# Performance work log

Hardware: AMD Instinct MI355X
Metric: run time of the kernel (lower is better)

Reference implementation:

```python
import jax, jax.numpy as jnp
import numpy as np

OUT, IN, R = 8192, 8192, 16
GROUP = 16
SCALING = 16.0 / 16.0  # lora_alpha / r
# nvfp4 (e2m1) code table: 3 low bits magnitude, bit 3 = sign
NVFP4_LUT = jnp.array([0.0, 0.5, 1.0, 1.5, 2.0, 3.0, 4.0, 6.0,
                       -0.0, -0.5, -1.0, -1.5, -2.0, -3.0, -4.0, -6.0],
                      dtype=jnp.float32)


def setup_inputs() -> dict:
    key = jax.random.key(0)
    k1, k2, k3, k4, k5 = jax.random.split(key, 5)
    x = jax.random.normal(k1, (64, IN), dtype=jnp.float32)
    packed_weight = jax.random.randint(k2, (OUT, IN // 2), 0, 256, dtype=jnp.int32).astype(jnp.uint8)
    # effective block scales (global scale already absorbed, as in _load_prequantized_nvfp4)
    weight_block_scales = (jax.random.uniform(k3, (OUT, IN // GROUP), dtype=jnp.float32) + 0.1) * 0.01
    lora_A = jax.random.normal(k4, (R, IN), dtype=jnp.float32) * (1.0 / np.sqrt(IN))
    lora_B = jax.random.normal(k5, (OUT, R), dtype=jnp.float32) * 0.01
    return {"x": x, "packed_weight": packed_weight,
            "weight_block_scales": weight_block_scales,
            "lora_A": lora_A, "lora_B": lora_B}


def _dequant_nvfp4(packed, block_scales):
    # packed: (OUT, IN//2) uint8, two fp4 codes per byte (low nibble = even index)
    low = (packed & 0xF).astype(jnp.int32)
    high = (packed >> 4).astype(jnp.int32)
    codes = jnp.stack([low, high], axis=-1).reshape(packed.shape[0], -1)  # (OUT, IN)
    vals = NVFP4_LUT[codes]
    O, I = vals.shape
    # per-block scale over groups of GROUP along in_features
    W = (vals.reshape(O, I // GROUP, GROUP) * block_scales[:, :, None]).reshape(O, I)
    return W


def reference(x, packed_weight, weight_block_scales, lora_A, lora_B):
    W = _dequant_nvfp4(packed_weight, weight_block_scales)      # (OUT, IN) fp32
    base = x @ W.T                                              # (B, OUT)
    lora = (x @ lora_A.T) @ lora_B.T                            # (B, OUT)
    return base + SCALING * lora
```

## Files before the change

kernel.cpp:

```cpp
#include <hip/hip_runtime.h>
#include <stdint.h>

#define IN_F   8192
#define OUT_F  8192
#define MB     64
#define RANK   16
#define KSPLIT 16

typedef _Float16 f16x8 __attribute__((ext_vector_type(8)));
typedef _Float16 f16x2 __attribute__((ext_vector_type(2)));
typedef float    f32x4 __attribute__((ext_vector_type(4)));

__device__ __forceinline__ unsigned pk2h(float a, float b) {
    return __builtin_bit_cast(unsigned, __builtin_amdgcn_cvt_pkrtz(a, b));
}

__device__ __forceinline__ f16x8 decode8(unsigned p, unsigned s2) {
    unsigned q  = p >> 4;
    unsigned me = __builtin_amdgcn_perm(0x46444240u, 0x3E3C3800u, p & 0x07070707u);
    unsigned mo = __builtin_amdgcn_perm(0x46444240u, 0x3E3C3800u, q & 0x07070707u);
    unsigned he = ((p & 0x08080808u) << 4) | me;
    unsigned ho = ((q & 0x08080808u) << 4) | mo;
    unsigned bu0 = __builtin_amdgcn_perm(ho, he, 0x040C000Cu);
    unsigned bu1 = __builtin_amdgcn_perm(ho, he, 0x050C010Cu);
    unsigned bu2 = __builtin_amdgcn_perm(ho, he, 0x060C020Cu);
    unsigned bu3 = __builtin_amdgcn_perm(ho, he, 0x070C030Cu);
    f16x2 sv = __builtin_bit_cast(f16x2, s2);
    f16x2 h0 = __builtin_bit_cast(f16x2, bu0) * sv;
    f16x2 h1 = __builtin_bit_cast(f16x2, bu1) * sv;
    f16x2 h2 = __builtin_bit_cast(f16x2, bu2) * sv;
    f16x2 h3 = __builtin_bit_cast(f16x2, bu3) * sv;
    f16x8 b;
    b[0]=h0[0]; b[1]=h0[1]; b[2]=h1[0]; b[3]=h1[1];
    b[4]=h2[0]; b[5]=h2[1]; b[6]=h3[0]; b[7]=h3[1];
    return b;
}

__device__ __forceinline__ unsigned pack4(uint4 a) {
    unsigned t0 = __builtin_amdgcn_perm(a.y, a.x, 0x0C0C0400u);
    unsigned t1 = __builtin_amdgcn_perm(a.w, a.z, 0x0C0C0400u);
    return __builtin_amdgcn_perm(t1, t0, 0x05040100u);
}

__global__ __launch_bounds__(256) void prep_kernel(
    const float* __restrict__ x, const float* __restrict__ lora_A,
    uint2* __restrict__ xf2, float* __restrict__ tp)
{
    const int m = blockIdx.x, kq = blockIdx.y;
    const int tid = threadIdx.x;
    const int mt = m >> 4, l15 = m & 15;
    float acc[RANK];
#pragma unroll
    for (int r = 0; r < RANK; ++r) acc[r] = 0.f;

    const float4* x4 = (const float4*)(x + (size_t)m * IN_F);
    const float4* A4 = (const float4*)lora_A;
#pragma unroll
    for (int it = 0; it < 2; ++it) {
        int j = kq * 512 + it * 256 + tid;
        float4 xv = x4[j];
        uint2 u;
        u.x = pk2h(xv.x, xv.y);
        u.y = pk2h(xv.z, xv.w);
        int kstep = j >> 3, quad = (j >> 1) & 3, h = j & 1;
        xf2[(size_t)(((kstep * 4 + mt) * 64 + quad * 16 + l15) * 2 + h)] = u;
#pragma unroll
        for (int r = 0; r < RANK; ++r) {
            float4 av = A4[(size_t)r * (IN_F / 4) + j];
            acc[r] += xv.x * av.x + xv.y * av.y + xv.z * av.z + xv.w * av.w;
        }
    }
#pragma unroll
    for (int r = 0; r < RANK; ++r)
#pragma unroll
        for (int off = 32; off > 0; off >>= 1)
            acc[r] += __shfl_down(acc[r], off);

    __shared__ float red[4][RANK];
    int lane = tid & 63, wid = tid >> 6;
    if (lane == 0) {
#pragma unroll
        for (int r = 0; r < RANK; ++r) red[wid][r] = acc[r];
    }
    __syncthreads();
    if (tid < RANK)
        tp[((size_t)kq * MB + m) * RANK + tid] =
            red[0][tid] + red[1][tid] + red[2][tid] + red[3][tid];
}

__device__ __forceinline__ float4 lora4(const float* __restrict__ tp, int m,
                                        const float* __restrict__ lora_B, int n4) {
    float ta[RANK];
#pragma unroll
    for (int r = 0; r < RANK; ++r) ta[r] = 0.f;
#pragma unroll
    for (int kq = 0; kq < 4; ++kq) {
        const float4* t4 = (const float4*)(tp + ((size_t)kq * MB + m) * RANK);
#pragma unroll
        for (int i = 0; i < 4; ++i) {
            float4 v = t4[i];
            ta[4*i+0] += v.x; ta[4*i+1] += v.y; ta[4*i+2] += v.z; ta[4*i+3] += v.w;
        }
    }
    float4 o;
    float* op = (float*)&o;
#pragma unroll
    for (int j = 0; j < 4; ++j) {
        const float4* B4 = (const float4*)(lora_B + (size_t)(n4 + j) * RANK);
        float s = 0.f;
#pragma unroll
        for (int i = 0; i < 4; ++i) {
            float4 b = B4[i];
            s += ta[4*i+0]*b.x + ta[4*i+1]*b.y + ta[4*i+2]*b.z + ta[4*i+3]*b.w;
        }
        op[j] = s;
    }
    return o;
}

__global__ __launch_bounds__(256) void lora_kernel(
    const float* __restrict__ tp, const float* __restrict__ lora_B,
    float* __restrict__ out)
{
    const int gid = blockIdx.x * 256 + threadIdx.x;
    ((float4*)out)[gid] = lora4(tp, gid >> 11, lora_B, (gid & 2047) * 4);
}

__global__ __launch_bounds__(256) void finish_kernel(
    const float* __restrict__ partial, const float* __restrict__ tp,
    const float* __restrict__ lora_B, float* __restrict__ out)
{
    const int gid = blockIdx.x * 256 + threadIdx.x;
    float4 p = {0.f, 0.f, 0.f, 0.f};
#pragma unroll
    for (int ksp = 0; ksp < KSPLIT; ++ksp) {
        float4 v = ((const float4*)partial)[(size_t)ksp * (MB * OUT_F / 4) + gid];
        p.x += v.x; p.y += v.y; p.z += v.z; p.w += v.w;
    }
    float4 l = lora4(tp, gid >> 11, lora_B, (gid & 2047) * 4);
    p.x += l.x; p.y += l.y; p.z += l.z; p.w += l.w;
    ((float4*)out)[gid] = p;
}

template<int ATOMIC>
__global__ __launch_bounds__(256, 3) void main4_kernel(
    const void*  __restrict__ Wpv,
    const float* __restrict__ scales,
    const uint4* __restrict__ xf4,
    float*       __restrict__ dst)
{
    __shared__ __align__(16) unsigned wbuf[2][2048];

    const int tid = threadIdx.x;
    const int lane = tid & 63, w = tid >> 6;
    const int l15 = lane & 15, quad = lane >> 4, qh = quad >> 1;
    const int ks = blockIdx.x, by = blockIdx.y;
    const int n0 = by * 128 + w * 32;
    const int row = n0 + l15;

    unsigned dv = ((const unsigned*)Wpv)[lane];
    const bool fmt1 = (__ballot(dv > 255u) == 0ull);

    unsigned sreg[2][16];
#pragma unroll
    for (int nt = 0; nt < 2; ++nt) {
        const float4* sp = (const float4*)(scales + (size_t)(row + nt * 16) * (IN_F / 16)
                                           + ks * 32);
#pragma unroll
        for (int i = 0; i < 8; ++i) {
            float4 vv = sp[i];
            float a = qh ? vv.y : vv.x, b = qh ? vv.w : vv.z;
            sreg[nt][2 * i]     = pk2h(a, a);
            sreg[nt][2 * i + 1] = pk2h(b, b);
        }
    }

    f32x4 acc[4][2];
#pragma unroll
    for (int mt = 0; mt < 4; ++mt)
#pragma unroll
        for (int nt = 0; nt < 2; ++nt)
            acc[mt][nt] = (f32x4){0.f, 0.f, 0.f, 0.f};

    const uint4* xp  = xf4 + (size_t)ks * 4096 + lane;
    const uint4* Wp4 = (const uint4*)Wpv;

    uint4 rg[8];

#define LOADC(c)                                                              \
    do {                                                                      \
        if (fmt1) {                                                           \
            _Pragma("unroll") for (int i = 0; i < 8; ++i) {                   \
                int rl = (tid >> 4) + i * 16;                                 \
                rg[i] = Wp4[(size_t)(by * 128 + rl) * 1024                    \
                            + (ks * 64 + (c) * 16 + (tid & 15))];             \
            }                                                                 \
        } else {                                                              \
            _Pragma("unroll") for (int i = 0; i < 2; ++i) {                   \
                int rl = (tid >> 2) + i * 64;                                 \
                rg[i] = Wp4[(size_t)(by * 128 + rl) * 256                     \
                            + (ks * 16 + (c) * 4 + (tid & 3))];               \
            }                                                                 \
        }                                                                     \
    } while (0)

#define WRITEC(buf)                                                           \
    do {                                                                      \
        if (fmt1) {                                                           \
            int te = tid & 15;                                                \
            _Pragma("unroll") for (int i = 0; i < 8; ++i) {                   \
                int rl = (tid >> 4) + i * 16;                                 \
                wbuf[buf][rl * 16 + (te ^ (rl & 14))] = pack4(rg[i]);         \
            }                                                                 \
        } else {                                                              \
            _Pragma("unroll") for (int i = 0; i < 2; ++i) {                   \
                int rl = (tid >> 2) + i * 64;                                 \
                int eb = (tid & 3) * 4;                                       \
                wbuf[buf][rl * 16 + ((eb + 0) ^ (rl & 14))] = rg[i].x;        \
                wbuf[buf][rl * 16 + ((eb + 1) ^ (rl & 14))] = rg[i].y;        \
                wbuf[buf][rl * 16 + ((eb + 2) ^ (rl & 14))] = rg[i].z;        \
                wbuf[buf][rl * 16 + ((eb + 3) ^ (rl & 14))] = rg[i].w;        \
            }                                                                 \
        }                                                                     \
    } while (0)

    LOADC(0);
    WRITEC(0);
    __syncthreads();
    LOADC(1);

#pragma unroll
    for (int c = 0; c < 4; ++c) {
#pragma unroll
        for (int sc = 0; sc < 4; ++sc) {
            const int s = c * 4 + sc;
            f16x8 afr[4];
#pragma unroll
            for (int mt = 0; mt < 4; ++mt)
                afr[mt] = __builtin_bit_cast(f16x8, xp[(s * 4 + mt) * 64]);
#pragma unroll
            for (int nt = 0; nt < 2; ++nt) {
                const int rl = w * 32 + nt * 16 + l15;
                unsigned p = wbuf[c & 1][rl * 16 + ((sc * 4 + quad) ^ (l15 & 14))];
                f16x8 b = decode8(p, sreg[nt][s]);
#pragma unroll
                for (int mt = 0; mt < 4; ++mt)
                    acc[mt][nt] = __builtin_amdgcn_mfma_f32_16x16x32_f16(
                        afr[mt], b, acc[mt][nt], 0, 0, 0);
            }
        }
        if (c < 3) {
            __syncthreads();
            WRITEC((c + 1) & 1);
            if (c < 2) LOADC(c + 2);
            __syncthreads();
        }
    }
#undef LOADC
#undef WRITEC

    if (ATOMIC == 0) {
        float* pb = dst + (size_t)ks * (MB * OUT_F);
#pragma unroll
        for (int mt = 0; mt < 4; ++mt)
#pragma unroll
            for (int nt = 0; nt < 2; ++nt)
#pragma unroll
                for (int r = 0; r < 4; ++r)
                    pb[(size_t)(mt * 16 + quad * 4 + r) * OUT_F + n0 + nt * 16 + l15]
                        = acc[mt][nt][r];
    } else {
#pragma unroll
        for (int mt = 0; mt < 4; ++mt)
#pragma unroll
            for (int nt = 0; nt < 2; ++nt)
#pragma unroll
                for (int r = 0; r < 4; ++r)
                    atomicAdd(&dst[(size_t)(mt * 16 + quad * 4 + r) * OUT_F
                                   + n0 + nt * 16 + l15], acc[mt][nt][r]);
    }
}

extern "C" void kernel_launch(void* const* d_in, const int* in_sizes, int n_in,
                              void* d_out, int out_size, void* d_ws, size_t ws_size,
                              hipStream_t stream)
{
    (void)in_sizes; (void)n_in; (void)out_size;
    const float* x      = (const float*)d_in[0];
    const void*  Wp     = (const void*)d_in[1];
    const float* scales = (const float*)d_in[2];
    const float* lora_A = (const float*)d_in[3];
    const float* lora_B = (const float*)d_in[4];
    float* out = (float*)d_out;

    char* ws = (char*)d_ws;
    float* tp      = (float*)ws;
    uint2* xf      = (uint2*)(ws + 65536);
    float* partial = (float*)(ws + (2u << 20));
    const bool full = ws_size >= ((size_t)34 << 20);

    prep_kernel<<<dim3(64, 4), 256, 0, stream>>>(x, lora_A, xf, tp);

    if (full) {
        main4_kernel<0><<<dim3(KSPLIT, 64), 256, 0, stream>>>(
            Wp, scales, (const uint4*)xf, partial);
        finish_kernel<<<(MB * OUT_F / 4) / 256, 256, 0, stream>>>(
            partial, tp, lora_B, out);
    } else {
        lora_kernel<<<(MB * OUT_F / 4) / 256, 256, 0, stream>>>(tp, lora_B, out);
        main4_kernel<1><<<dim3(KSPLIT, 64), 256, 0, stream>>>(
            Wp, scales, (const uint4*)xf, out);
    }
}
```

Before: 239.8 us.

## Stage activations in LDS and use per-wave weight buffers without block barriers

The kernel now copies the block's whole activation slice into shared memory once, so the MMA loop reads A fragments from LDS instead of global memory. Each wave loads, repacks and reads its own weight rows through a private double-buffered LDS region. This removes the block-wide __syncthreads in the K loop and relies on manual s_waitcnt with two register stages to overlap loads. LDS use rises to about 80KB per block and the launch bound drops to 2 blocks per CU, cutting occupancy. The hand-coded waitcnt values and the lack of intra-wave LDS sync risk subtle ordering bugs.

After: 235.3 us. Within noise of the previous version (-1.9%).

```diff
diff --git a/kernel.cpp b/kernel.cpp
--- a/kernel.cpp
+++ b/kernel.cpp
@@ -14,6 +14,8 @@
 __device__ __forceinline__ unsigned pk2h(float a, float b) {
     return __builtin_bit_cast(unsigned, __builtin_amdgcn_cvt_pkrtz(a, b));
 }
+
+#define MEMBAR() __asm__ __volatile__("" ::: "memory")
 
 __device__ __forceinline__ f16x8 decode8(unsigned p, unsigned s2) {
     unsigned q  = p >> 4;
@@ -143,13 +145,14 @@
 }
 
 template<int ATOMIC>
-__global__ __launch_bounds__(256, 3) void main4_kernel(
+__global__ __launch_bounds__(256, 2) void main5_kernel(
     const void*  __restrict__ Wpv,
     const float* __restrict__ scales,
     const uint4* __restrict__ xf4,
     float*       __restrict__ dst)
 {
-    __shared__ __align__(16) unsigned wbuf[2][2048];
+    __shared__ __align__(16) uint4    xs[4096];
+    __shared__ __align__(16) unsigned wpk[4][2][512];
 
     const int tid = threadIdx.x;
     const int lane = tid & 63, w = tid >> 6;
@@ -175,89 +178,110 @@
         }
     }
 
-    f32x4 acc[4][2];
-#pragma unroll
-    for (int mt = 0; mt < 4; ++mt)
-#pragma unroll
-        for (int nt = 0; nt < 2; ++nt)
-            acc[mt][nt] = (f32x4){0.f, 0.f, 0.f, 0.f};
-
-    const uint4* xp  = xf4 + (size_t)ks * 4096 + lane;
     const uint4* Wp4 = (const uint4*)Wpv;
-
-    uint4 rg[8];
-
-#define LOADC(c)                                                              \
+    uint4 rg[2][8];
+
+#define LOADW(c, p)                                                           \
     do {                                                                      \
         if (fmt1) {                                                           \
             _Pragma("unroll") for (int i = 0; i < 8; ++i) {                   \
-                int rl = (tid >> 4) + i * 16;                                 \
-                rg[i] = Wp4[(size_t)(by * 128 + rl) * 1024                    \
-                            + (ks * 64 + (c) * 16 + (tid & 15))];             \
+                int idx = i * 64 + lane;                                      \
+                int r = idx >> 4, col = idx & 15;                             \
+                rg[p][i] = Wp4[(size_t)(n0 + r) * 1024                        \
+                               + (ks * 64 + (c) * 16 + col)];                 \
             }                                                                 \
         } else {                                                              \
             _Pragma("unroll") for (int i = 0; i < 2; ++i) {                   \
-                int rl = (tid >> 2) + i * 64;                                 \
-                rg[i] = Wp4[(size_t)(by * 128 + rl) * 256                     \
-                            + (ks * 16 + (c) * 4 + (tid & 3))];               \
+                int idx = i * 64 + lane;                                      \
+                int r = idx >> 2, u = idx & 3;                                \
+                rg[p][i] = Wp4[(size_t)(n0 + r) * 256                         \
+                               + (ks * 16 + (c) * 4 + u)];                    \
             }                                                                 \
         }                                                                     \
     } while (0)
 
-#define WRITEC(buf)                                                           \
+#define WRITEW(c, p)                                                          \
     do {                                                                      \
+        unsigned* wb = &wpk[w][(c) & 1][0];                                   \
         if (fmt1) {                                                           \
-            int te = tid & 15;                                                \
             _Pragma("unroll") for (int i = 0; i < 8; ++i) {                   \
-                int rl = (tid >> 4) + i * 16;                                 \
-                wbuf[buf][rl * 16 + (te ^ (rl & 14))] = pack4(rg[i]);         \
+                int idx = i * 64 + lane;                                      \
+                int r = idx >> 4, dcol = idx & 15;                            \
+                wb[r * 16 + (dcol & 3) * 4 + (dcol >> 2)] = pack4(rg[p][i]);  \
             }                                                                 \
         } else {                                                              \
             _Pragma("unroll") for (int i = 0; i < 2; ++i) {                   \
-                int rl = (tid >> 2) + i * 64;                                 \
-                int eb = (tid & 3) * 4;                                       \
-                wbuf[buf][rl * 16 + ((eb + 0) ^ (rl & 14))] = rg[i].x;        \
-                wbuf[buf][rl * 16 + ((eb + 1) ^ (rl & 14))] = rg[i].y;        \
-                wbuf[buf][rl * 16 + ((eb + 2) ^ (rl & 14))] = rg[i].z;        \
-                wbuf[buf][rl * 16 + ((eb + 3) ^ (rl & 14))] = rg[i].w;        \
+                int idx = i * 64 + lane;                                      \
+                int r = idx >> 2, u = idx & 3;                                \
+                wb[r * 16 + 0 * 4 + u] = rg[p][i].x;                          \
+                wb[r * 16 + 1 * 4 + u] = rg[p][i].y;                          \
+                wb[r * 16 + 2 * 4 + u] = rg[p][i].z;                          \
+                wb[r * 16 + 3 * 4 + u] = rg[p][i].w;                          \
             }                                                                 \
         }                                                                     \
     } while (0)
 
-    LOADC(0);
-    WRITEC(0);
+    uint4 xr[16];
+    {
+        const uint4* gsrc = xf4 + (size_t)ks * 4096;
+#pragma unroll
+        for (int i = 0; i < 16; ++i) xr[i] = gsrc[i * 256 + tid];
+    }
+    LOADW(0, 0);
+    LOADW(1, 1);
+#pragma unroll
+    for (int i = 0; i < 16; ++i) xs[i * 256 + tid] = xr[i];
     __syncthreads();
-    LOADC(1);
+
+    f32x4 acc[4][2];
+#pragma unroll
+    for (int mt = 0; mt < 4; ++mt)
+#pragma unroll
+        for (int nt = 0; nt < 2; ++nt)
+            acc[mt][nt] = (f32x4){0.f, 0.f, 0.f, 0.f};
+
+    MEMBAR();
+    __builtin_amdgcn_s_waitcnt(0x0F78);
+    MEMBAR();
+    WRITEW(0, 0);
 
 #pragma unroll
     for (int c = 0; c < 4; ++c) {
+        const uint4* wb4 = (const uint4*)&wpk[w][c & 1][0];
+        uint4 b0 = wb4[(0 * 16 + l15) * 4 + quad];
+        uint4 b1 = wb4[(1 * 16 + l15) * 4 + quad];
 #pragma unroll
         for (int sc = 0; sc < 4; ++sc) {
             const int s = c * 4 + sc;
             f16x8 afr[4];
 #pragma unroll
             for (int mt = 0; mt < 4; ++mt)
-                afr[mt] = __builtin_bit_cast(f16x8, xp[(s * 4 + mt) * 64]);
-#pragma unroll
-            for (int nt = 0; nt < 2; ++nt) {
-                const int rl = w * 32 + nt * 16 + l15;
-                unsigned p = wbuf[c & 1][rl * 16 + ((sc * 4 + quad) ^ (l15 & 14))];
-                f16x8 b = decode8(p, sreg[nt][s]);
-#pragma unroll
-                for (int mt = 0; mt < 4; ++mt)
-                    acc[mt][nt] = __builtin_amdgcn_mfma_f32_16x16x32_f16(
-                        afr[mt], b, acc[mt][nt], 0, 0, 0);
-            }
+                afr[mt] = __builtin_bit_cast(f16x8, xs[(s * 4 + mt) * 64 + lane]);
+            const unsigned pw0 = sc == 0 ? b0.x : sc == 1 ? b0.y : sc == 2 ? b0.z : b0.w;
+            const unsigned pw1 = sc == 0 ? b1.x : sc == 1 ? b1.y : sc == 2 ? b1.z : b1.w;
+            f16x8 bb0 = decode8(pw0, sreg[0][s]);
+#pragma unroll
+            for (int mt = 0; mt < 4; ++mt)
+                acc[mt][0] = __builtin_amdgcn_mfma_f32_16x16x32_f16(
+                    afr[mt], bb0, acc[mt][0], 0, 0, 0);
+            f16x8 bb1 = decode8(pw1, sreg[1][s]);
+#pragma unroll
+            for (int mt = 0; mt < 4; ++mt)
+                acc[mt][1] = __builtin_amdgcn_mfma_f32_16x16x32_f16(
+                    afr[mt], bb1, acc[mt][1], 0, 0, 0);
         }
         if (c < 3) {
-            __syncthreads();
-            WRITEC((c + 1) & 1);
-            if (c < 2) LOADC(c + 2);
-            __syncthreads();
-        }
-    }
-#undef LOADC
-#undef WRITEC
+            MEMBAR();
+            if (c < 2) LOADW(c + 2, c & 1);
+            MEMBAR();
+            if (c < 2) { __builtin_amdgcn_s_waitcnt(0x0F78); }
+            else       { __builtin_amdgcn_s_waitcnt(0x0F70); }
+            MEMBAR();
+            WRITEW(c + 1, (c + 1) & 1);
+        }
+    }
+#undef LOADW
+#undef WRITEW
 
     if (ATOMIC == 0) {
         float* pb = dst + (size_t)ks * (MB * OUT_F);
@@ -302,13 +326,13 @@
     prep_kernel<<<dim3(64, 4), 256, 0, stream>>>(x, lora_A, xf, tp);
 
     if (full) {
-        main4_kernel<0><<<dim3(KSPLIT, 64), 256, 0, stream>>>(
+        main5_kernel<0><<<dim3(KSPLIT, 64), 256, 0, stream>>>(
             Wp, scales, (const uint4*)xf, partial);
         finish_kernel<<<(MB * OUT_F / 4) / 256, 256, 0, stream>>>(
             partial, tp, lora_B, out);
     } else {
         lora_kernel<<<(MB * OUT_F / 4) / 256, 256, 0, stream>>>(tp, lora_B, out);
-        main4_kernel<1><<<dim3(KSPLIT, 64), 256, 0, stream>>>(
+        main5_kernel<1><<<dim3(KSPLIT, 64), 256, 0, stream>>>(
             Wp, scales, (const uint4*)xf, out);
     }
 }
```

## Restructure main kernel: whole K-slab in LDS, fewer k-splits, narrower N tiles

Applied to the files above, without the earlier changes.

The main kernel now splits K only four ways. Each block covers 64 output rows and loads its full 2048-wide K slab of packed weights and block scales into LDS in one pass, replacing the double-buffered chunk pipeline. Each wave computes one 16-column N tile over 64 MFMA steps, and scales are read per step from LDS rather than held in registers. This cuts partial-sum workspace and finish-kernel reduction traffic by a factor of four, at the cost of about 80KB of LDS per block, no overlap between weight loading and compute, and lower occupancy.

Result: no change. 236.6 us (-1.3%).

```diff
diff --git a/kernel.cpp b/kernel.cpp
--- a/kernel.cpp
+++ b/kernel.cpp
@@ -5,7 +5,7 @@
 #define OUT_F  8192
 #define MB     64
 #define RANK   16
-#define KSPLIT 16
+#define KSPLIT 4
 
 typedef _Float16 f16x8 __attribute__((ext_vector_type(8)));
 typedef _Float16 f16x2 __attribute__((ext_vector_type(2)));
@@ -143,141 +143,100 @@
 }
 
 template<int ATOMIC>
-__global__ __launch_bounds__(256, 3) void main4_kernel(
+__global__ __launch_bounds__(256, 2) void main6_kernel(
     const void*  __restrict__ Wpv,
     const float* __restrict__ scales,
     const uint4* __restrict__ xf4,
     float*       __restrict__ dst)
 {
-    __shared__ __align__(16) unsigned wbuf[2][2048];
+    __shared__ __align__(16) unsigned wlds[64 * 256];
+    __shared__ __align__(16) unsigned slds[64 * 64];
 
     const int tid = threadIdx.x;
     const int lane = tid & 63, w = tid >> 6;
     const int l15 = lane & 15, quad = lane >> 4, qh = quad >> 1;
-    const int ks = blockIdx.x, by = blockIdx.y;
-    const int n0 = by * 128 + w * 32;
-    const int row = n0 + l15;
+    const int ksp = blockIdx.x, by = blockIdx.y;
+    const int nb = by * 64;
+    const int rw = w * 16 + l15;
 
     unsigned dv = ((const unsigned*)Wpv)[lane];
     const bool fmt1 = (__ballot(dv > 255u) == 0ull);
 
-    unsigned sreg[2][16];
-#pragma unroll
-    for (int nt = 0; nt < 2; ++nt) {
-        const float4* sp = (const float4*)(scales + (size_t)(row + nt * 16) * (IN_F / 16)
-                                           + ks * 32);
-#pragma unroll
-        for (int i = 0; i < 8; ++i) {
-            float4 vv = sp[i];
-            float a = qh ? vv.y : vv.x, b = qh ? vv.w : vv.z;
-            sreg[nt][2 * i]     = pk2h(a, a);
-            sreg[nt][2 * i + 1] = pk2h(b, b);
-        }
-    }
-
-    f32x4 acc[4][2];
-#pragma unroll
-    for (int mt = 0; mt < 4; ++mt)
-#pragma unroll
-        for (int nt = 0; nt < 2; ++nt)
-            acc[mt][nt] = (f32x4){0.f, 0.f, 0.f, 0.f};
-
-    const uint4* xp  = xf4 + (size_t)ks * 4096 + lane;
     const uint4* Wp4 = (const uint4*)Wpv;
 
-    uint4 rg[8];
-
-#define LOADC(c)                                                              \
-    do {                                                                      \
-        if (fmt1) {                                                           \
-            _Pragma("unroll") for (int i = 0; i < 8; ++i) {                   \
-                int rl = (tid >> 4) + i * 16;                                 \
-                rg[i] = Wp4[(size_t)(by * 128 + rl) * 1024                    \
-                            + (ks * 64 + (c) * 16 + (tid & 15))];             \
-            }                                                                 \
-        } else {                                                              \
-            _Pragma("unroll") for (int i = 0; i < 2; ++i) {                   \
-                int rl = (tid >> 2) + i * 64;                                 \
-                rg[i] = Wp4[(size_t)(by * 128 + rl) * 256                     \
-                            + (ks * 16 + (c) * 4 + (tid & 3))];               \
-            }                                                                 \
-        }                                                                     \
-    } while (0)
-
-#define WRITEC(buf)                                                           \
-    do {                                                                      \
-        if (fmt1) {                                                           \
-            int te = tid & 15;                                                \
-            _Pragma("unroll") for (int i = 0; i < 8; ++i) {                   \
-                int rl = (tid >> 4) + i * 16;                                 \
-                wbuf[buf][rl * 16 + (te ^ (rl & 14))] = pack4(rg[i]);         \
-            }                                                                 \
-        } else {                                                              \
-            _Pragma("unroll") for (int i = 0; i < 2; ++i) {                   \
-                int rl = (tid >> 2) + i * 64;                                 \
-                int eb = (tid & 3) * 4;                                       \
-                wbuf[buf][rl * 16 + ((eb + 0) ^ (rl & 14))] = rg[i].x;        \
-                wbuf[buf][rl * 16 + ((eb + 1) ^ (rl & 14))] = rg[i].y;        \
-                wbuf[buf][rl * 16 + ((eb + 2) ^ (rl & 14))] = rg[i].z;        \
-                wbuf[buf][rl * 16 + ((eb + 3) ^ (rl & 14))] = rg[i].w;        \
-            }                                                                 \
-        }                                                                     \
-    } while (0)
-
-    LOADC(0);
-    WRITEC(0);
+    if (fmt1) {
+#pragma unroll 4
+        for (int r = 0; r < 64; ++r) {
+            uint4 a = Wp4[(size_t)(nb + r) * 1024 + ksp * 256 + tid];
+            wlds[r * 256 + (tid ^ ((r & 7) << 2))] = pack4(a);
+        }
+    } else {
+#pragma unroll 4
+        for (int r = 0; r < 16; ++r) {
+            int seg = r * 256 + tid;
+            int row = seg >> 6, c16 = seg & 63;
+            uint4 a = Wp4[(size_t)(nb + row) * 256 + ksp * 64 + c16];
+            int base = row * 256, swz = (row & 7) << 2;
+            wlds[base + ((c16 * 4 + 0) ^ swz)] = a.x;
+            wlds[base + ((c16 * 4 + 1) ^ swz)] = a.y;
+            wlds[base + ((c16 * 4 + 2) ^ swz)] = a.z;
+            wlds[base + ((c16 * 4 + 3) ^ swz)] = a.w;
+        }
+    }
+
+#pragma unroll
+    for (int r = 0; r < 8; ++r) {
+        int seg = r * 256 + tid;
+        int row = seg >> 5, u = seg & 31;
+        float4 v = ((const float4*)(scales + (size_t)(nb + row) * (IN_F / 16)
+                                    + ksp * 128))[u];
+        int base = row * 64, swz = (row & 7) << 2;
+        slds[base + ((2 * u + 0) ^ swz)] = pk2h(v.x, v.y);
+        slds[base + ((2 * u + 1) ^ swz)] = pk2h(v.z, v.w);
+    }
     __syncthreads();
-    LOADC(1);
-
-#pragma unroll
-    for (int c = 0; c < 4; ++c) {
-#pragma unroll
-        for (int sc = 0; sc < 4; ++sc) {
-            const int s = c * 4 + sc;
-            f16x8 afr[4];
-#pragma unroll
-            for (int mt = 0; mt < 4; ++mt)
-                afr[mt] = __builtin_bit_cast(f16x8, xp[(s * 4 + mt) * 64]);
-#pragma unroll
-            for (int nt = 0; nt < 2; ++nt) {
-                const int rl = w * 32 + nt * 16 + l15;
-                unsigned p = wbuf[c & 1][rl * 16 + ((sc * 4 + quad) ^ (l15 & 14))];
-                f16x8 b = decode8(p, sreg[nt][s]);
-#pragma unroll
-                for (int mt = 0; mt < 4; ++mt)
-                    acc[mt][nt] = __builtin_amdgcn_mfma_f32_16x16x32_f16(
-                        afr[mt], b, acc[mt][nt], 0, 0, 0);
-            }
-        }
-        if (c < 3) {
-            __syncthreads();
-            WRITEC((c + 1) & 1);
-            if (c < 2) LOADC(c + 2);
-            __syncthreads();
-        }
-    }
-#undef LOADC
-#undef WRITEC
-
+
+    f32x4 acc[4];
+#pragma unroll
+    for (int mt = 0; mt < 4; ++mt) acc[mt] = (f32x4){0.f, 0.f, 0.f, 0.f};
+
+    const unsigned* wrow = &wlds[rw * 256];
+    const unsigned* srow = &slds[rw * 64];
+    const int wswz = (rw & 7) << 2;
+    const unsigned ssel = qh ? 0x03020302u : 0x01000100u;
+    const uint4* xp = xf4 + (size_t)ksp * (64 * 4 * 64) + lane;
+
+#pragma unroll 16
+    for (int s = 0; s < 64; ++s) {
+        f16x8 afr[4];
+#pragma unroll
+        for (int mt = 0; mt < 4; ++mt)
+            afr[mt] = __builtin_bit_cast(f16x8, xp[(s * 4 + mt) * 64]);
+        unsigned p  = wrow[(s * 4 + quad) ^ wswz];
+        unsigned sd = srow[s ^ wswz];
+        unsigned s2 = __builtin_amdgcn_perm(sd, sd, ssel);
+        f16x8 b = decode8(p, s2);
+#pragma unroll
+        for (int mt = 0; mt < 4; ++mt)
+            acc[mt] = __builtin_amdgcn_mfma_f32_16x16x32_f16(
+                afr[mt], b, acc[mt], 0, 0, 0);
+    }
+
+    const int ncol = nb + w * 16 + l15;
     if (ATOMIC == 0) {
-        float* pb = dst + (size_t)ks * (MB * OUT_F);
-#pragma unroll
-        for (int mt = 0; mt < 4; ++mt)
-#pragma unroll
-            for (int nt = 0; nt < 2; ++nt)
-#pragma unroll
-                for (int r = 0; r < 4; ++r)
-                    pb[(size_t)(mt * 16 + quad * 4 + r) * OUT_F + n0 + nt * 16 + l15]
-                        = acc[mt][nt][r];
+        float* pb = dst + (size_t)ksp * (MB * OUT_F);
+#pragma unroll
+        for (int mt = 0; mt < 4; ++mt)
+#pragma unroll
+            for (int r = 0; r < 4; ++r)
+                pb[(size_t)(mt * 16 + quad * 4 + r) * OUT_F + ncol] = acc[mt][r];
     } else {
 #pragma unroll
         for (int mt = 0; mt < 4; ++mt)
 #pragma unroll
-            for (int nt = 0; nt < 2; ++nt)
-#pragma unroll
-                for (int r = 0; r < 4; ++r)
-                    atomicAdd(&dst[(size_t)(mt * 16 + quad * 4 + r) * OUT_F
-                                   + n0 + nt * 16 + l15], acc[mt][nt][r]);
+            for (int r = 0; r < 4; ++r)
+                atomicAdd(&dst[(size_t)(mt * 16 + quad * 4 + r) * OUT_F + ncol],
+                          acc[mt][r]);
     }
 }
 
@@ -297,18 +256,18 @@
     float* tp      = (float*)ws;
     uint2* xf      = (uint2*)(ws + 65536);
     float* partial = (float*)(ws + (2u << 20));
-    const bool full = ws_size >= ((size_t)34 << 20);
+    const bool full = ws_size >= ((size_t)12 << 20);
 
     prep_kernel<<<dim3(64, 4), 256, 0, stream>>>(x, lora_A, xf, tp);
 
     if (full) {
-        main4_kernel<0><<<dim3(KSPLIT, 64), 256, 0, stream>>>(
+        main6_kernel<0><<<dim3(KSPLIT, 128), 256, 0, stream>>>(
             Wp, scales, (const uint4*)xf, partial);
         finish_kernel<<<(MB * OUT_F / 4) / 256, 256, 0, stream>>>(
             partial, tp, lora_B, out);
     } else {
         lora_kernel<<<(MB * OUT_F / 4) / 256, 256, 0, stream>>>(tp, lora_B, out);
-        main4_kernel<1><<<dim3(KSPLIT, 64), 256, 0, stream>>>(
+        main6_kernel<1><<<dim3(KSPLIT, 128), 256, 0, stream>>>(
             Wp, scales, (const uint4*)xf, out);
     }
 }
```

## Stage activations in LDS and give each wave a private weight tile

Applied to the files above, without the earlier changes.

The main GEMM kernel now runs 512-thread blocks, each covering 256 output rows instead of 128, and launches half as many blocks. Each block loads its activation slice (x split) into shared memory once. Each wave stages its own 32-row weight tile in two halves, swizzled per wave, so the per-chunk block-wide barriers of the old kernel go away. The aim is to cut repeated global reads of x and the barrier overhead, at the cost of much more LDS per block (64KB x plus 64KB weights), which may limit occupancy.

Result: faster. 233.9 us (-2.5%).

```diff
diff --git a/kernel.cpp b/kernel.cpp
--- a/kernel.cpp
+++ b/kernel.cpp
@@ -143,29 +143,77 @@
 }
 
 template<int ATOMIC>
-__global__ __launch_bounds__(256, 3) void main4_kernel(
+__global__ __launch_bounds__(512, 2) void main7_kernel(
     const void*  __restrict__ Wpv,
     const float* __restrict__ scales,
     const uint4* __restrict__ xf4,
     float*       __restrict__ dst)
 {
-    __shared__ __align__(16) unsigned wbuf[2][2048];
+    __shared__ __align__(16) uint4    xs[4096];
+    __shared__ __align__(16) unsigned wlds[8][32][64];
 
     const int tid = threadIdx.x;
     const int lane = tid & 63, w = tid >> 6;
     const int l15 = lane & 15, quad = lane >> 4, qh = quad >> 1;
     const int ks = blockIdx.x, by = blockIdx.y;
-    const int n0 = by * 128 + w * 32;
-    const int row = n0 + l15;
+    const int n0 = by * 256 + w * 32;
+    const int lr8 = lane >> 3, lc8 = lane & 7;
+    const int lr2 = lane >> 1, lc2 = lane & 1;
 
     unsigned dv = ((const unsigned*)Wpv)[lane];
     const bool fmt1 = (__ballot(dv > 255u) == 0ull);
 
+    const uint4* Wp4 = (const uint4*)Wpv;
+    uint4 lt[16];
+
+#define LOADW(h)                                                              \
+    do {                                                                      \
+        if (fmt1) {                                                           \
+            _Pragma("unroll") for (int p = 0; p < 4; ++p)                     \
+            _Pragma("unroll") for (int i = 0; i < 4; ++i)                     \
+                lt[p * 4 + i] = Wp4[(size_t)(n0 + p * 8 + lr8) * 1024         \
+                                    + ks * 64 + (h) * 32 + i * 8 + lc8];      \
+        } else {                                                              \
+            _Pragma("unroll") for (int i = 0; i < 4; ++i)                     \
+                lt[i] = Wp4[(size_t)(n0 + lr2) * 256                          \
+                            + ks * 16 + (h) * 8 + i * 2 + lc2];              \
+        }                                                                     \
+    } while (0)
+
+#define WRITEW(h)                                                             \
+    do {                                                                      \
+        if (fmt1) {                                                           \
+            _Pragma("unroll") for (int p = 0; p < 4; ++p) {                   \
+                int rl = p * 8 + lr8, sw = (rl & 7) << 2;                     \
+                _Pragma("unroll") for (int i = 0; i < 4; ++i)                 \
+                    wlds[w][rl][((h) * 32 + i * 8 + lc8) ^ sw]                \
+                        = pack4(lt[p * 4 + i]);                               \
+            }                                                                 \
+        } else {                                                              \
+            int rl = lr2, sw = (rl & 7) << 2;                                 \
+            _Pragma("unroll") for (int i = 0; i < 4; ++i) {                   \
+                int d0 = ((h) * 8 + i * 2 + lc2) * 4;                         \
+                wlds[w][rl][(d0 + 0) ^ sw] = lt[i].x;                         \
+                wlds[w][rl][(d0 + 1) ^ sw] = lt[i].y;                         \
+                wlds[w][rl][(d0 + 2) ^ sw] = lt[i].z;                         \
+                wlds[w][rl][(d0 + 3) ^ sw] = lt[i].w;                         \
+            }                                                                 \
+        }                                                                     \
+    } while (0)
+
+    uint4 xr[8];
+    {
+        const uint4* gsrc = xf4 + (size_t)ks * 4096;
+#pragma unroll
+        for (int i = 0; i < 8; ++i) xr[i] = gsrc[i * 512 + tid];
+    }
+    LOADW(0);
+
     unsigned sreg[2][16];
 #pragma unroll
     for (int nt = 0; nt < 2; ++nt) {
-        const float4* sp = (const float4*)(scales + (size_t)(row + nt * 16) * (IN_F / 16)
-                                           + ks * 32);
+        const float4* sp = (const float4*)(scales
+                           + (size_t)(n0 + nt * 16 + l15) * (IN_F / 16) + ks * 32);
 #pragma unroll
         for (int i = 0; i < 8; ++i) {
             float4 vv = sp[i];
@@ -175,6 +223,11 @@
         }
     }
 
+#pragma unroll
+    for (int i = 0; i < 8; ++i) xs[i * 512 + tid] = xr[i];
+    WRITEW(0);
+    __syncthreads();
+
     f32x4 acc[4][2];
 #pragma unroll
     for (int mt = 0; mt < 4; ++mt)
@@ -182,82 +235,33 @@
         for (int nt = 0; nt < 2; ++nt)
             acc[mt][nt] = (f32x4){0.f, 0.f, 0.f, 0.f};
 
-    const uint4* xp  = xf4 + (size_t)ks * 4096 + lane;
-    const uint4* Wp4 = (const uint4*)Wpv;
-
-    uint4 rg[8];
-
-#define LOADC(c)                                                              \
+    LOADW(1);
+
+#define COMPUTE(h)                                                            \
     do {                                                                      \
-        if (fmt1) {                                                           \
-            _Pragma("unroll") for (int i = 0; i < 8; ++i) {                   \
-                int rl = (tid >> 4) + i * 16;                                 \
-                rg[i] = Wp4[(size_t)(by * 128 + rl) * 1024                    \
-                            + (ks * 64 + (c) * 16 + (tid & 15))];             \
-            }                                                                 \
-        } else {                                                              \
-            _Pragma("unroll") for (int i = 0; i < 2; ++i) {                   \
-                int rl = (tid >> 2) + i * 64;                                 \
-                rg[i] = Wp4[(size_t)(by * 128 + rl) * 256                     \
-                            + (ks * 16 + (c) * 4 + (tid & 3))];               \
+        _Pragma("unroll") for (int sc = 0; sc < 8; ++sc) {                    \
+            const int s = (h) * 8 + sc;                                       \
+            f16x8 afr[4];                                                     \
+            _Pragma("unroll") for (int mt = 0; mt < 4; ++mt)                  \
+                afr[mt] = __builtin_bit_cast(f16x8, xs[(s * 4 + mt) * 64 + lane]); \
+            _Pragma("unroll") for (int nt = 0; nt < 2; ++nt) {                \
+                int rl = nt * 16 + l15;                                       \
+                unsigned p = wlds[w][rl][(s * 4 + quad) ^ ((rl & 7) << 2)];   \
+                f16x8 b = decode8(p, sreg[nt][s]);                            \
+                _Pragma("unroll") for (int mt = 0; mt < 4; ++mt)              \
+                    acc[mt][nt] = __builtin_amdgcn_mfma_f32_16x16x32_f16(     \
+                        afr[mt], b, acc[mt][nt], 0, 0, 0);                    \
             }                                                                 \
         }                                                                     \
     } while (0)
 
-#define WRITEC(buf)                                                           \
-    do {                                                                      \
-        if (fmt1) {                                                           \
-            int te = tid & 15;                                                \
-            _Pragma("unroll") for (int i = 0; i < 8; ++i) {                   \
-                int rl = (tid >> 4) + i * 16;                                 \
-                wbuf[buf][rl * 16 + (te ^ (rl & 14))] = pack4(rg[i]);         \
-            }                                                                 \
-        } else {                                                              \
-            _Pragma("unroll") for (int i = 0; i < 2; ++i) {                   \
-                int rl = (tid >> 2) + i * 64;                                 \
-                int eb = (tid & 3) * 4;                                       \
-                wbuf[buf][rl * 16 + ((eb + 0) ^ (rl & 14))] = rg[i].x;        \
-                wbuf[buf][rl * 16 + ((eb + 1) ^ (rl & 14))] = rg[i].y;        \
-                wbuf[buf][rl * 16 + ((eb + 2) ^ (rl & 14))] = rg[i].z;        \
-                wbuf[buf][rl * 16 + ((eb + 3) ^ (rl & 14))] = rg[i].w;        \
-            }                                                                 \
-        }                                                                     \
-    } while (0)
-
-    LOADC(0);
-    WRITEC(0);
-    __syncthreads();
-    LOADC(1);
-
-#pragma unroll
-    for (int c = 0; c < 4; ++c) {
-#pragma unroll
-        for (int sc = 0; sc < 4; ++sc) {
-            const int s = c * 4 + sc;
-            f16x8 afr[4];
-#pragma unroll
-            for (int mt = 0; mt < 4; ++mt)
-                afr[mt] = __builtin_bit_cast(f16x8, xp[(s * 4 + mt) * 64]);
-#pragma unroll
-            for (int nt = 0; nt < 2; ++nt) {
-                const int rl = w * 32 + nt * 16 + l15;
-                unsigned p = wbuf[c & 1][rl * 16 + ((sc * 4 + quad) ^ (l15 & 14))];
-                f16x8 b = decode8(p, sreg[nt][s]);
-#pragma unroll
-                for (int mt = 0; mt < 4; ++mt)
-                    acc[mt][nt] = __builtin_amdgcn_mfma_f32_16x16x32_f16(
-                        afr[mt], b, acc[mt][nt], 0, 0, 0);
-            }
-        }
-        if (c < 3) {
-            __syncthreads();
-            WRITEC((c + 1) & 1);
-            if (c < 2) LOADC(c + 2);
-            __syncthreads();
-        }
-    }
-#undef LOADC
-#undef WRITEC
+    COMPUTE(0);
+    WRITEW(1);
+    COMPUTE(1);
+
+#undef LOADW
+#undef WRITEW
+#undef COMPUTE
 
     if (ATOMIC == 0) {
         float* pb = dst + (size_t)ks * (MB * OUT_F);
@@ -267,8 +271,8 @@
             for (int nt = 0; nt < 2; ++nt)
 #pragma unroll
                 for (int r = 0; r < 4; ++r)
-                    pb[(size_t)(mt * 16 + quad * 4 + r) * OUT_F + n0 + nt * 16 + l15]
-                        = acc[mt][nt][r];
+                    pb[(size_t)(mt * 16 + quad * 4 + r) * OUT_F
+                       + n0 + nt * 16 + l15] = acc[mt][nt][r];
     } else {
 #pragma unroll
         for (int mt = 0; mt < 4; ++mt)
@@ -302,13 +306,13 @@
     prep_kernel<<<dim3(64, 4), 256, 0, stream>>>(x, lora_A, xf, tp);
 
     if (full) {
-        main4_kernel<0><<<dim3(KSPLIT, 64), 256, 0, stream>>>(
+        main7_kernel<0><<<dim3(KSPLIT, 32), 512, 0, stream>>>(
             Wp, scales, (const uint4*)xf, partial);
         finish_kernel<<<(MB * OUT_F / 4) / 256, 256, 0, stream>>>(
             partial, tp, lora_B, out);
     } else {
         lora_kernel<<<(MB * OUT_F / 4) / 256, 256, 0, stream>>>(tp, lora_B, out);
-        main4_kernel<1><<<dim3(KSPLIT, 64), 256, 0, stream>>>(
+        main7_kernel<1><<<dim3(KSPLIT, 32), 512, 0, stream>>>(
             Wp, scales, (const uint4*)xf, out);
     }
 }
```
